# Performance work log

Hardware: AMD Instinct MI355X
Metric: run time of the kernel (lower is better)

## Reference

```python
import jax, jax.numpy as jnp
import numpy as np

N_NEURON = 500_000
N_EDGE = 10_000_000
TAO_D = 2.0
TAO_R = 10.0
DT = 0.1
LAMDA_D = DT / TAO_D  # dt/tao_d
LAMDA_R = DT / TAO_R  # dt/tao_r


def setup_inputs() -> dict:
    key = jax.random.key(0)
    ks = jax.random.split(key, 8)
    edges = jax.random.randint(ks[0], (2, N_EDGE), 0, N_NEURON, dtype=jnp.int64)  # row0=post, row1=pre
    return {
        "weight": jax.random.normal(ks[1], (N_EDGE,), dtype=jnp.float32),
        "edges": edges,
        "Iback": jax.random.normal(ks[2], (N_NEURON,), dtype=jnp.float32),
        "spike": jax.random.uniform(ks[3], (N_NEURON,), dtype=jnp.float32),
        "s": jax.random.normal(ks[4], (N_NEURON,), dtype=jnp.float32),
        "r": jax.random.normal(ks[5], (N_NEURON,), dtype=jnp.float32),
        "noise": jax.random.normal(ks[6], (N_NEURON,), dtype=jnp.float32),
        "dt_over_tau": jax.random.uniform(ks[7], (1,), dtype=jnp.float32),
        "sqrt_coeff": jnp.ones((1,), dtype=jnp.float32),
        "sig": jnp.ones((1,), dtype=jnp.float32),
        "mu": jnp.zeros((1,), dtype=jnp.float32),
    }


def reference(weight, edges, Iback, spike, s, r, noise, dt_over_tau, sqrt_coeff, sig, mu):
    # OU background-current update + effective input current
    Iback_new = Iback + dt_over_tau * (noise - Iback)
    Ieff = Iback_new / sqrt_coeff * sig + mu
    # dual-exponential synaptic trace updates
    s_new = s + LAMDA_R * (-s + spike / TAO_D)
    r_new = r - LAMDA_D * r + DT * s_new
    # sparse COO matvec: I[post] += w_e * r_new[pre]
    post, pre = edges[0], edges[1]
    I = jax.ops.segment_sum(weight * r_new[pre], post, num_segments=N_NEURON) + Ieff
    return I
```

## Files before the change

kernel.cpp:

```cpp
#include <hip/hip_runtime.h>
#include <hip/hip_fp16.h>

#define N_NEURON 500000
#define N_EDGE   10000000

#define DT_C      0.1f
#define LAMDA_D_C 0.05f
#define LAMDA_R_C 0.01f
#define INV_TAO_D 0.5f

#define BUCKET_SHIFT 11
#define BUCKET_W     (1 << BUCKET_SHIFT)
#define NBUCKET      ((N_NEURON + BUCKET_W - 1) >> BUCKET_SHIFT)

#define P1_BLOCK 256
#define P1_EPT   16
#define P1_CHUNK (P1_BLOCK * P1_EPT)
#define NCHUNK   ((N_EDGE + P1_CHUNK - 1) / P1_CHUNK)
#define OFFS_STRIDE 256

#define WS_RNEW_OFF  0u
#define WS_OFFS_OFF  (2u * 1024u * 1024u)
#define WS_REC_OFF   (8u * 1024u * 1024u)
#define WS_NEEDED    ((size_t)WS_REC_OFF + (size_t)NCHUNK * P1_CHUNK * 4u)

__device__ __forceinline__ unsigned pack_rec(int post, float v) {
    const unsigned short hv = __half_as_ushort(__float2half_rn(v));
    return ((unsigned)hv << 16) | ((unsigned)post & (BUCKET_W - 1));
}
__device__ __forceinline__ float rec_val(unsigned rec) {
    return __half2float(__ushort_as_half((unsigned short)(rec >> 16)));
}

__global__ void neuron_update_r(const float4* __restrict__ spike,
                                const float4* __restrict__ s,
                                const float4* __restrict__ r,
                                float4* __restrict__ r_new,
                                int n4) {
    const int i = blockIdx.x * blockDim.x + threadIdx.x;
    if (i >= n4) return;
    const float4 sv = s[i], sp = spike[i], rv = r[i];
    float4 rn;
    float sn;
    sn = sv.x + LAMDA_R_C * (-sv.x + sp.x * INV_TAO_D); rn.x = rv.x - LAMDA_D_C * rv.x + DT_C * sn;
    sn = sv.y + LAMDA_R_C * (-sv.y + sp.y * INV_TAO_D); rn.y = rv.y - LAMDA_D_C * rv.y + DT_C * sn;
    sn = sv.z + LAMDA_R_C * (-sv.z + sp.z * INV_TAO_D); rn.z = rv.z - LAMDA_D_C * rv.z + DT_C * sn;
    sn = sv.w + LAMDA_R_C * (-sv.w + sp.w * INV_TAO_D); rn.w = rv.w - LAMDA_D_C * rv.w + DT_C * sn;
    r_new[i] = rn;
}

__global__ __launch_bounds__(P1_BLOCK, 8) void edge_bin(
        const float* __restrict__ weight,
        const int*   __restrict__ post_arr,
        const int*   __restrict__ pre_arr,
        const float* __restrict__ r_new,
        unsigned*    __restrict__ records,
        unsigned*    __restrict__ offs,
        int n_edge) {
    __shared__ unsigned rec_lds[P1_CHUNK];
    __shared__ unsigned cnt[NBUCKET];
    __shared__ unsigned lbase[NBUCKET + 1];
    __shared__ unsigned lfill[NBUCKET];

    const int t      = threadIdx.x;
    const int chunk0 = blockIdx.x * P1_CHUNK;

    for (int i = t; i < NBUCKET; i += P1_BLOCK) cnt[i] = 0;
    __syncthreads();

    {
        int4 P[4];
        #pragma unroll
        for (int k = 0; k < 4; ++k) {
            const int e = chunk0 + (k * P1_BLOCK + t) * 4;
            P[k] = (e < n_edge) ? *reinterpret_cast<const int4*>(post_arr + e)
                                : make_int4(-1, -1, -1, -1);
        }
        #pragma unroll
        for (int k = 0; k < 4; ++k) {
            if (P[k].x >= 0) {
                atomicAdd(&cnt[((unsigned)P[k].x) >> BUCKET_SHIFT], 1u);
                atomicAdd(&cnt[((unsigned)P[k].y) >> BUCKET_SHIFT], 1u);
                atomicAdd(&cnt[((unsigned)P[k].z) >> BUCKET_SHIFT], 1u);
                atomicAdd(&cnt[((unsigned)P[k].w) >> BUCKET_SHIFT], 1u);
            }
        }
    }
    __syncthreads();

    if (t < 64) {
        unsigned carry = 0;
        #pragma unroll
        for (int c = 0; c < 4; ++c) {
            const int idx = c * 64 + t;
            unsigned v = (idx < NBUCKET) ? cnt[idx] : 0u;
            const unsigned orig = v;
            #pragma unroll
            for (int d = 1; d < 64; d <<= 1) {
                const unsigned u = __shfl_up(v, d);
                if (t >= d) v += u;
            }
            if (idx <= NBUCKET) {
                const unsigned ex = carry + v - orig;
                lbase[idx] = ex;
                if (idx < NBUCKET) lfill[idx] = ex;
            }
            carry += __shfl(v, 63);
        }
    }
    __syncthreads();

    if (t <= NBUCKET)
        offs[blockIdx.x * OFFS_STRIDE + t] = lbase[t];

    #pragma unroll
    for (int h = 0; h < 2; ++h) {
        int4   P[2], Q[2];
        float4 W[2];
        #pragma unroll
        for (int k = 0; k < 2; ++k) {
            const int e = chunk0 + ((h * 2 + k) * P1_BLOCK + t) * 4;
            if (e < n_edge) {
                P[k] = *reinterpret_cast<const int4*>(post_arr + e);
                Q[k] = *reinterpret_cast<const int4*>(pre_arr + e);
                W[k] = *reinterpret_cast<const float4*>(weight + e);
            } else {
                P[k] = make_int4(-1, -1, -1, -1);
                Q[k] = make_int4(0, 0, 0, 0);
                W[k] = make_float4(0.f, 0.f, 0.f, 0.f);
            }
        }
        float g[8];
        #pragma unroll
        for (int k = 0; k < 2; ++k) {
            g[k * 4 + 0] = r_new[Q[k].x];
            g[k * 4 + 1] = r_new[Q[k].y];
            g[k * 4 + 2] = r_new[Q[k].z];
            g[k * 4 + 3] = r_new[Q[k].w];
        }
        unsigned slot[8], rec[8];
        #pragma unroll
        for (int k = 0; k < 2; ++k) {
            const int   ps[4] = {P[k].x, P[k].y, P[k].z, P[k].w};
            const float wv[4] = {W[k].x, W[k].y, W[k].z, W[k].w};
            #pragma unroll
            for (int j = 0; j < 4; ++j) {
                const int m = k * 4 + j;
                if (ps[j] >= 0) {
                    slot[m] = atomicAdd(&lfill[((unsigned)ps[j]) >> BUCKET_SHIFT], 1u);
                    rec[m]  = pack_rec(ps[j], wv[j] * g[m]);
                } else {
                    slot[m] = 0xFFFFFFFFu;
                }
            }
        }
        #pragma unroll
        for (int m = 0; m < 8; ++m)
            if (slot[m] != 0xFFFFFFFFu) rec_lds[slot[m]] = rec[m];
    }
    __syncthreads();

    const unsigned total = lbase[NBUCKET];
    unsigned* dst = records + (size_t)blockIdx.x * P1_CHUNK;
    for (unsigned i = t; i < total; i += P1_BLOCK)
        dst[i] = rec_lds[i];
}

__global__ __launch_bounds__(1024) void bucket_reduce(
        const unsigned* __restrict__ records,
        const unsigned* __restrict__ offs,
        const float* __restrict__ Iback,
        const float* __restrict__ noise,
        const float* __restrict__ dt_over_tau,
        const float* __restrict__ sqrt_coeff,
        const float* __restrict__ sig,
        const float* __restrict__ mu,
        float*          __restrict__ out,
        int n, int nchunk) {
    __shared__ float acc[BUCKET_W];
    const int b = blockIdx.x;
    const int t = threadIdx.x;
    for (int i = t; i < BUCKET_W; i += 1024) acc[i] = 0.f;
    __syncthreads();

    const int grp = t >> 4, lane = t & 15;
    for (int j = grp; j < nchunk; j += 64) {
        const unsigned s0 = offs[j * OFFS_STRIDE + b];
        const unsigned e0 = offs[j * OFFS_STRIDE + b + 1];
        const unsigned* src = records + (size_t)j * P1_CHUNK;
        for (unsigned i = s0 + lane; i < e0; i += 16) {
            const unsigned rec = src[i];
            atomicAdd(&acc[rec & (BUCKET_W - 1)], rec_val(rec));
        }
    }
    __syncthreads();

    const float dtau = dt_over_tau[0];
    const float sq   = sqrt_coeff[0];
    const float sg   = sig[0];
    const float m    = mu[0];
    const int g0 = b << BUCKET_SHIFT;
    for (int i = t; i < BUCKET_W; i += 1024) {
        const int g = g0 + i;
        if (g < n) {
            const float ib  = Iback[g];
            const float ibn = ib + dtau * (noise[g] - ib);
            out[g] = acc[i] + (ibn / sq * sg + m);
        }
    }
}

__global__ void neuron_update_full(const float* __restrict__ Iback,
                                   const float* __restrict__ spike,
                                   const float* __restrict__ s,
                                   const float* __restrict__ r,
                                   const float* __restrict__ noise,
                                   const float* __restrict__ dt_over_tau,
                                   const float* __restrict__ sqrt_coeff,
                                   const float* __restrict__ sig,
                                   const float* __restrict__ mu,
                                   float* __restrict__ r_new,
                                   float* __restrict__ out,
                                   int n) {
    const float dtau = dt_over_tau[0], sq = sqrt_coeff[0], sg = sig[0], m = mu[0];
    for (int i = blockIdx.x * blockDim.x + threadIdx.x; i < n;
         i += gridDim.x * blockDim.x) {
        float ib  = Iback[i];
        float ibn = ib + dtau * (noise[i] - ib);
        float sv  = s[i];
        float sn  = sv + LAMDA_R_C * (-sv + spike[i] * INV_TAO_D);
        float rv  = r[i];
        r_new[i] = rv - LAMDA_D_C * rv + DT_C * sn;
        out[i]   = ibn / sq * sg + m;
    }
}

__global__ void edge_scatter(const float* __restrict__ weight,
                             const int* __restrict__ post,
                             const int* __restrict__ pre,
                             const float* __restrict__ r_new,
                             float* __restrict__ out,
                             int n_edge) {
    for (int e = blockIdx.x * blockDim.x + threadIdx.x; e < n_edge;
         e += gridDim.x * blockDim.x) {
        atomicAdd(&out[post[e]], weight[e] * r_new[pre[e]]);
    }
}

extern "C" void kernel_launch(void* const* d_in, const int* in_sizes, int n_in,
                              void* d_out, int out_size, void* d_ws, size_t ws_size,
                              hipStream_t stream) {
    const float* weight      = (const float*)d_in[0];
    const int*   edges       = (const int*)d_in[1];
    const float* Iback       = (const float*)d_in[2];
    const float* spike       = (const float*)d_in[3];
    const float* s           = (const float*)d_in[4];
    const float* r           = (const float*)d_in[5];
    const float* noise       = (const float*)d_in[6];
    const float* dt_over_tau = (const float*)d_in[7];
    const float* sqrt_coeff  = (const float*)d_in[8];
    const float* sig         = (const float*)d_in[9];
    const float* mu          = (const float*)d_in[10];

    float* out = (float*)d_out;
    char*  ws  = (char*)d_ws;

    float*    r_new   = (float*)(ws + WS_RNEW_OFF);
    unsigned* offs    = (unsigned*)(ws + WS_OFFS_OFF);
    unsigned* records = (unsigned*)(ws + WS_REC_OFF);

    const int n_edge = in_sizes[0];
    const int n      = out_size;

    const int nchunk = (n_edge + P1_CHUNK - 1) / P1_CHUNK;

    if (ws_size >= WS_NEEDED) {
        {
            const int n4 = n / 4;
            neuron_update_r<<<(n4 + 255) / 256, 256, 0, stream>>>(
                (const float4*)spike, (const float4*)s, (const float4*)r,
                (float4*)r_new, n4);
        }
        edge_bin<<<nchunk, P1_BLOCK, 0, stream>>>(
            weight, edges, edges + n_edge, r_new, records, offs, n_edge);

        bucket_reduce<<<NBUCKET, 1024, 0, stream>>>(
            records, offs, Iback, noise, dt_over_tau, sqrt_coeff, sig, mu,
            out, n, nchunk);
    } else {
        neuron_update_full<<<(n + 255) / 256, 256, 0, stream>>>(
            Iback, spike, s, r, noise, dt_over_tau, sqrt_coeff, sig, mu,
            r_new, out, n);
        edge_scatter<<<4096, 256, 0, stream>>>(
            weight, edges, edges + n_edge, r_new, out, n_edge);
    }
}
```

Baseline: 125.6 us.

## Split edge gather from binning into separate gather_pack kernel with fp16 staging

Moves the random r_new gather and weight multiply out of the LDS-heavy binning kernel into a standalone grid-stride kernel that writes the products as packed fp16 into a workspace buffer. The binning kernel then reads only post indices and the packed values. The aim is to decouple latency-bound random gathers from the occupancy-limited binning kernel. In exchange it adds an extra global write and read of 20 MB plus another kernel launch.

Result: slower. 135.3 us (+7.7%).

```diff
diff --git a/kernel.cpp b/kernel.cpp
--- a/kernel.cpp
+++ b/kernel.cpp
@@ -20,14 +20,11 @@
 #define OFFS_STRIDE 256
 
 #define WS_RNEW_OFF  0u
-#define WS_OFFS_OFF  (2u * 1024u * 1024u)
-#define WS_REC_OFF   (8u * 1024u * 1024u)
+#define WS_VH_OFF    (2u * 1024u * 1024u)
+#define WS_OFFS_OFF  (22u * 1024u * 1024u)
+#define WS_REC_OFF   (28u * 1024u * 1024u)
 #define WS_NEEDED    ((size_t)WS_REC_OFF + (size_t)NCHUNK * P1_CHUNK * 4u)
 
-__device__ __forceinline__ unsigned pack_rec(int post, float v) {
-    const unsigned short hv = __half_as_ushort(__float2half_rn(v));
-    return ((unsigned)hv << 16) | ((unsigned)post & (BUCKET_W - 1));
-}
 __device__ __forceinline__ float rec_val(unsigned rec) {
     return __half2float(__ushort_as_half((unsigned short)(rec >> 16)));
 }
@@ -49,13 +46,43 @@
     r_new[i] = rn;
 }
 
-__global__ __launch_bounds__(P1_BLOCK, 8) void edge_bin(
+__global__ __launch_bounds__(256) void gather_pack(
         const float* __restrict__ weight,
-        const int*   __restrict__ post_arr,
         const int*   __restrict__ pre_arr,
         const float* __restrict__ r_new,
-        unsigned*    __restrict__ records,
-        unsigned*    __restrict__ offs,
+        uint4*       __restrict__ vh,
+        int n_edge) {
+    const int tid    = blockIdx.x * blockDim.x + threadIdx.x;
+    const int stride = gridDim.x * blockDim.x;
+    const int niter  = n_edge >> 3;
+    for (int it = tid; it < niter; it += stride) {
+        const int e = it << 3;
+        const int4   q0 = *reinterpret_cast<const int4*>(pre_arr + e);
+        const int4   q1 = *reinterpret_cast<const int4*>(pre_arr + e + 4);
+        const float4 w0 = *reinterpret_cast<const float4*>(weight + e);
+        const float4 w1 = *reinterpret_cast<const float4*>(weight + e + 4);
+        float g[8];
+        g[0] = r_new[q0.x]; g[1] = r_new[q0.y]; g[2] = r_new[q0.z]; g[3] = r_new[q0.w];
+        g[4] = r_new[q1.x]; g[5] = r_new[q1.y]; g[6] = r_new[q1.z]; g[7] = r_new[q1.w];
+        const float wv[8] = {w0.x, w0.y, w0.z, w0.w, w1.x, w1.y, w1.z, w1.w};
+        unsigned h[8];
+        #pragma unroll
+        for (int j = 0; j < 8; ++j)
+            h[j] = (unsigned)__half_as_ushort(__float2half_rn(wv[j] * g[j]));
+        uint4 outv;
+        outv.x = h[0] | (h[1] << 16);
+        outv.y = h[2] | (h[3] << 16);
+        outv.z = h[4] | (h[5] << 16);
+        outv.w = h[6] | (h[7] << 16);
+        vh[it] = outv;
+    }
+}
+
+__global__ __launch_bounds__(P1_BLOCK, 8) void sort_bin(
+        const int*      __restrict__ post_arr,
+        const unsigned* __restrict__ vh,
+        unsigned*       __restrict__ records,
+        unsigned*       __restrict__ offs,
         int n_edge) {
     __shared__ unsigned rec_lds[P1_CHUNK];
     __shared__ unsigned cnt[NBUCKET];
@@ -115,40 +142,31 @@
 
     #pragma unroll
     for (int h = 0; h < 2; ++h) {
-        int4   P[2], Q[2];
-        float4 W[2];
+        int4  P[2];
+        uint2 V[2];
         #pragma unroll
         for (int k = 0; k < 2; ++k) {
             const int e = chunk0 + ((h * 2 + k) * P1_BLOCK + t) * 4;
             if (e < n_edge) {
                 P[k] = *reinterpret_cast<const int4*>(post_arr + e);
-                Q[k] = *reinterpret_cast<const int4*>(pre_arr + e);
-                W[k] = *reinterpret_cast<const float4*>(weight + e);
+                V[k] = *reinterpret_cast<const uint2*>(vh + (e >> 1));
             } else {
                 P[k] = make_int4(-1, -1, -1, -1);
-                Q[k] = make_int4(0, 0, 0, 0);
-                W[k] = make_float4(0.f, 0.f, 0.f, 0.f);
-            }
-        }
-        float g[8];
+                V[k] = make_uint2(0u, 0u);
+            }
+        }
+        unsigned slot[8], rec[8];
         #pragma unroll
         for (int k = 0; k < 2; ++k) {
-            g[k * 4 + 0] = r_new[Q[k].x];
-            g[k * 4 + 1] = r_new[Q[k].y];
-            g[k * 4 + 2] = r_new[Q[k].z];
-            g[k * 4 + 3] = r_new[Q[k].w];
-        }
-        unsigned slot[8], rec[8];
-        #pragma unroll
-        for (int k = 0; k < 2; ++k) {
-            const int   ps[4] = {P[k].x, P[k].y, P[k].z, P[k].w};
-            const float wv[4] = {W[k].x, W[k].y, W[k].z, W[k].w};
+            const int      ps[4] = {P[k].x, P[k].y, P[k].z, P[k].w};
+            const unsigned hv[4] = {V[k].x & 0xFFFFu, V[k].x >> 16,
+                                    V[k].y & 0xFFFFu, V[k].y >> 16};
             #pragma unroll
             for (int j = 0; j < 4; ++j) {
                 const int m = k * 4 + j;
                 if (ps[j] >= 0) {
                     slot[m] = atomicAdd(&lfill[((unsigned)ps[j]) >> BUCKET_SHIFT], 1u);
-                    rec[m]  = pack_rec(ps[j], wv[j] * g[m]);
+                    rec[m]  = (hv[j] << 16) | ((unsigned)ps[j] & (BUCKET_W - 1));
                 } else {
                     slot[m] = 0xFFFFFFFFu;
                 }
@@ -266,6 +284,7 @@
     char*  ws  = (char*)d_ws;
 
     float*    r_new   = (float*)(ws + WS_RNEW_OFF);
+    unsigned* vh      = (unsigned*)(ws + WS_VH_OFF);
     unsigned* offs    = (unsigned*)(ws + WS_OFFS_OFF);
     unsigned* records = (unsigned*)(ws + WS_REC_OFF);
 
@@ -281,8 +300,11 @@
                 (const float4*)spike, (const float4*)s, (const float4*)r,
                 (float4*)r_new, n4);
         }
-        edge_bin<<<nchunk, P1_BLOCK, 0, stream>>>(
-            weight, edges, edges + n_edge, r_new, records, offs, n_edge);
+        gather_pack<<<2048, 256, 0, stream>>>(
+            weight, edges + n_edge, r_new, (uint4*)vh, n_edge);
+
+        sort_bin<<<nchunk, P1_BLOCK, 0, stream>>>(
+            edges, vh, records, offs, n_edge);
 
         bucket_reduce<<<NBUCKET, 1024, 0, stream>>>(
             records, offs, Iback, noise, dt_over_tau, sqrt_coeff, sig, mu,
```

## Load all edge data up front and overlap gathers with bucket counting

Applied to the files above, without the earlier changes.

Edge_bin now loads post, weight and pre for all 16 edges per thread at the start, and issues the random r_new gathers before the counting barrier and prefix scan. The goal is to hide gather latency behind the histogram and scan work instead of taking two serialized load phases afterwards. The launch-bounds occupancy hint is lowered from 8 to 4 to allow more registers, and the copy-out uses 128-bit stores. Holding many more values in registers may reduce occupancy. The vector store path assumes total is a multiple of 4, otherwise it reads LDS beyond total and writes past it in the block's record slot.

After: 125.9 us. No clear change (+0.2%).

```diff
diff --git a/kernel.cpp b/kernel.cpp
--- a/kernel.cpp
+++ b/kernel.cpp
@@ -24,10 +24,6 @@
 #define WS_REC_OFF   (8u * 1024u * 1024u)
 #define WS_NEEDED    ((size_t)WS_REC_OFF + (size_t)NCHUNK * P1_CHUNK * 4u)
 
-__device__ __forceinline__ unsigned pack_rec(int post, float v) {
-    const unsigned short hv = __half_as_ushort(__float2half_rn(v));
-    return ((unsigned)hv << 16) | ((unsigned)post & (BUCKET_W - 1));
-}
 __device__ __forceinline__ float rec_val(unsigned rec) {
     return __half2float(__ushort_as_half((unsigned short)(rec >> 16)));
 }
@@ -49,7 +45,7 @@
     r_new[i] = rn;
 }
 
-__global__ __launch_bounds__(P1_BLOCK, 8) void edge_bin(
+__global__ __launch_bounds__(P1_BLOCK, 4) void edge_bin(
         const float* __restrict__ weight,
         const int*   __restrict__ post_arr,
         const int*   __restrict__ pre_arr,
@@ -68,23 +64,45 @@
     for (int i = t; i < NBUCKET; i += P1_BLOCK) cnt[i] = 0;
     __syncthreads();
 
-    {
-        int4 P[4];
-        #pragma unroll
-        for (int k = 0; k < 4; ++k) {
-            const int e = chunk0 + (k * P1_BLOCK + t) * 4;
-            P[k] = (e < n_edge) ? *reinterpret_cast<const int4*>(post_arr + e)
-                                : make_int4(-1, -1, -1, -1);
-        }
-        #pragma unroll
-        for (int k = 0; k < 4; ++k) {
-            if (P[k].x >= 0) {
-                atomicAdd(&cnt[((unsigned)P[k].x) >> BUCKET_SHIFT], 1u);
-                atomicAdd(&cnt[((unsigned)P[k].y) >> BUCKET_SHIFT], 1u);
-                atomicAdd(&cnt[((unsigned)P[k].z) >> BUCKET_SHIFT], 1u);
-                atomicAdd(&cnt[((unsigned)P[k].w) >> BUCKET_SHIFT], 1u);
-            }
-        }
+    int4   P[4];
+    float4 W[4];
+    int4   Q[4];
+    #pragma unroll
+    for (int k = 0; k < 4; ++k) {
+        const int e = chunk0 + (k * P1_BLOCK + t) * 4;
+        P[k] = (e < n_edge) ? *reinterpret_cast<const int4*>(post_arr + e)
+                            : make_int4(-1, -1, -1, -1);
+    }
+    #pragma unroll
+    for (int k = 0; k < 4; ++k) {
+        const int e = chunk0 + (k * P1_BLOCK + t) * 4;
+        W[k] = (e < n_edge) ? *reinterpret_cast<const float4*>(weight + e)
+                            : make_float4(0.f, 0.f, 0.f, 0.f);
+    }
+    #pragma unroll
+    for (int k = 0; k < 4; ++k) {
+        const int e = chunk0 + (k * P1_BLOCK + t) * 4;
+        Q[k] = (e < n_edge) ? *reinterpret_cast<const int4*>(pre_arr + e)
+                            : make_int4(0, 0, 0, 0);
+    }
+
+    #pragma unroll
+    for (int k = 0; k < 4; ++k) {
+        if (P[k].x >= 0) {
+            atomicAdd(&cnt[((unsigned)P[k].x) >> BUCKET_SHIFT], 1u);
+            atomicAdd(&cnt[((unsigned)P[k].y) >> BUCKET_SHIFT], 1u);
+            atomicAdd(&cnt[((unsigned)P[k].z) >> BUCKET_SHIFT], 1u);
+            atomicAdd(&cnt[((unsigned)P[k].w) >> BUCKET_SHIFT], 1u);
+        }
+    }
+
+    float g[16];
+    #pragma unroll
+    for (int k = 0; k < 4; ++k) {
+        g[k * 4 + 0] = r_new[Q[k].x];
+        g[k * 4 + 1] = r_new[Q[k].y];
+        g[k * 4 + 2] = r_new[Q[k].z];
+        g[k * 4 + 3] = r_new[Q[k].w];
     }
     __syncthreads();
 
@@ -113,57 +131,43 @@
     if (t <= NBUCKET)
         offs[blockIdx.x * OFFS_STRIDE + t] = lbase[t];
 
-    #pragma unroll
-    for (int h = 0; h < 2; ++h) {
-        int4   P[2], Q[2];
-        float4 W[2];
+    unsigned slot[16];
+    #pragma unroll
+    for (int k = 0; k < 4; ++k) {
+        const int ps[4] = {P[k].x, P[k].y, P[k].z, P[k].w};
         #pragma unroll
-        for (int k = 0; k < 2; ++k) {
-            const int e = chunk0 + ((h * 2 + k) * P1_BLOCK + t) * 4;
-            if (e < n_edge) {
-                P[k] = *reinterpret_cast<const int4*>(post_arr + e);
-                Q[k] = *reinterpret_cast<const int4*>(pre_arr + e);
-                W[k] = *reinterpret_cast<const float4*>(weight + e);
-            } else {
-                P[k] = make_int4(-1, -1, -1, -1);
-                Q[k] = make_int4(0, 0, 0, 0);
-                W[k] = make_float4(0.f, 0.f, 0.f, 0.f);
+        for (int j = 0; j < 4; ++j) {
+            slot[k * 4 + j] = (ps[j] >= 0)
+                ? atomicAdd(&lfill[((unsigned)ps[j]) >> BUCKET_SHIFT], 1u)
+                : 0xFFFFFFFFu;
+        }
+    }
+
+    #pragma unroll
+    for (int k = 0; k < 4; ++k) {
+        const int   ps[4] = {P[k].x, P[k].y, P[k].z, P[k].w};
+        const float wv[4] = {W[k].x, W[k].y, W[k].z, W[k].w};
+        #pragma unroll
+        for (int j = 0; j < 4; ++j) {
+            const int m = k * 4 + j;
+            if (slot[m] != 0xFFFFFFFFu) {
+                const unsigned hv = (unsigned)__half_as_ushort(
+                    __float2half_rn(wv[j] * g[m]));
+                rec_lds[slot[m]] = (hv << 16) |
+                                   ((unsigned)ps[j] & (BUCKET_W - 1));
             }
         }
-        float g[8];
-        #pragma unroll
-        for (int k = 0; k < 2; ++k) {
-            g[k * 4 + 0] = r_new[Q[k].x];
-            g[k * 4 + 1] = r_new[Q[k].y];
-            g[k * 4 + 2] = r_new[Q[k].z];
-            g[k * 4 + 3] = r_new[Q[k].w];
-        }
-        unsigned slot[8], rec[8];
-        #pragma unroll
-        for (int k = 0; k < 2; ++k) {
-            const int   ps[4] = {P[k].x, P[k].y, P[k].z, P[k].w};
-            const float wv[4] = {W[k].x, W[k].y, W[k].z, W[k].w};
-            #pragma unroll
-            for (int j = 0; j < 4; ++j) {
-                const int m = k * 4 + j;
-                if (ps[j] >= 0) {
-                    slot[m] = atomicAdd(&lfill[((unsigned)ps[j]) >> BUCKET_SHIFT], 1u);
-                    rec[m]  = pack_rec(ps[j], wv[j] * g[m]);
-                } else {
-                    slot[m] = 0xFFFFFFFFu;
-                }
-            }
-        }
-        #pragma unroll
-        for (int m = 0; m < 8; ++m)
-            if (slot[m] != 0xFFFFFFFFu) rec_lds[slot[m]] = rec[m];
     }
     __syncthreads();
 
     const unsigned total = lbase[NBUCKET];
-    unsigned* dst = records + (size_t)blockIdx.x * P1_CHUNK;
-    for (unsigned i = t; i < total; i += P1_BLOCK)
-        dst[i] = rec_lds[i];
+    uint4* dst4 = reinterpret_cast<uint4*>(records + (size_t)blockIdx.x * P1_CHUNK);
+    for (unsigned i = t * 4; i < total; i += P1_BLOCK * 4) {
+        uint4 v;
+        v.x = rec_lds[i];     v.y = rec_lds[i + 1];
+        v.z = rec_lds[i + 2]; v.w = rec_lds[i + 3];
+        dst4[i >> 2] = v;
+    }
 }
 
 __global__ __launch_bounds__(1024) void bucket_reduce(
```
